# Performance work log

Hardware: AMD Instinct MI355X
Metric: run time of the kernel (lower is better)

## Reference

```python
import jax, jax.numpy as jnp
import numpy as np

MAXLEN = 256          # max per-graph segment length (static for jit)
SOFT_LABEL_NUM = 4    # hardcoded in the original module
B = 512               # num_graphs


def setup_inputs() -> dict:
    key = jax.random.key(0)
    k1, k2, k3 = jax.random.split(key, 3)
    # ragged per-graph lengths in [2, MAXLEN]; >=2 so the original's
    # length-1 skip path (and its cursor bug) never triggers
    s_num = jax.random.randint(k1, (B,), 2, MAXLEN + 1, dtype=jnp.int32)
    T = int(jnp.sum(s_num))
    logits = jax.random.normal(k2, (T,), dtype=jnp.float32)
    labels = jax.random.randint(k3, (T,), 0, SOFT_LABEL_NUM, dtype=jnp.int32)
    return {"logits": logits, "labels": labels, "s_num": s_num}


def reference(logits, labels, s_num):
    T = logits.shape[0]
    ends = jnp.cumsum(s_num)
    offsets = ends - s_num                                   # segment starts
    pos_in_seg = jnp.arange(MAXLEN)
    idx = jnp.clip(offsets[:, None] + pos_in_seg[None, :], 0, T - 1)  # [B, L]
    tok_mask = pos_in_seg[None, :] < s_num[:, None]                    # [B, L]

    lg = logits[idx]                                   # [B, L] padded logits
    lb = labels[idx]                                   # [B, L] padded labels

    # pairwise logsigmoid(pos - neg), computed once for all soft labels
    ls = jax.nn.log_sigmoid(lg[:, :, None] - lg[:, None, :])  # [B, L, L]

    means, valids = [], []
    for s in range(1, SOFT_LABEL_NUM):
        pos = (tok_mask & (lb == s)).astype(lg.dtype)  # [B, L]
        neg = (tok_mask & (lb < s)).astype(lg.dtype)   # [B, L]
        npos = pos.sum(-1)                             # [B]
        nneg = neg.sum(-1)                             # [B]
        pair_sum = jnp.einsum('bp,bpn,bn->b', pos, ls, neg)
        valid = (npos > 0) & (nneg > 0)
        mean_s = jnp.where(valid, pair_sum / jnp.maximum(npos * nneg, 1.0), 0.0)
        means.append(mean_s)
        valids.append(valid)

    means = jnp.stack(means)                 # [3, B]
    valids = jnp.stack(valids)               # [3, B]
    cnt = valids.astype(lg.dtype).sum(0)     # valid soft-label count per graph
    graph_valid = (s_num > 1) & (cnt > 0)
    graph_lp = jnp.where(graph_valid, means.sum(0) / jnp.maximum(cnt, 1.0), 0.0)
    n_valid = jnp.maximum(graph_valid.astype(lg.dtype).sum(), 1.0)
    loss = -(graph_lp.sum() / n_valid)
    return loss
```

## Files before the change

### kernel.cpp

```cpp
#include <hip/hip_runtime.h>
#include <hip/hip_bf16.h>


#define TAGHI 0xC0FFEE42u

__global__ __launch_bounds__(512) void bpr_one(const float* __restrict__ logits,
                                               const int* __restrict__ labels,
                                               const int* __restrict__ s_num,
                                               int B,
                                               unsigned long long* __restrict__ slot,
                                               float* __restrict__ out) {
    const int g    = blockIdx.x;
    const int t    = threadIdx.x;
    const int r    = t & 255;
    const int sl   = t >> 8;
    const int w    = t >> 6;
    const int lane = t & 63;

    __shared__ __align__(16) float se[256];
    __shared__ float sx[256];
    __shared__ float psum[4];
    __shared__ int   wcnt[4][4];
    __shared__ int   wpart[8];

    if (t < 4) psum[t] = 0.0f;

    int partial = 0;
    for (int i = t; i < g; i += 512) partial += s_num[i];
    #pragma unroll
    for (int off = 32; off > 0; off >>= 1)
        partial += __shfl_down(partial, off, 64);
    if (lane == 0) wpart[w] = partial;
    __syncthreads();
    int offset = 0;
    #pragma unroll
    for (int k = 0; k < 8; ++k) offset += wpart[k];
    const int L = s_num[g];

    float x = 0.0f;
    int   l = -1;
    if (t < 256 && t < L) {
        x = logits[offset + t];
        l = labels[offset + t];
    }
    const unsigned long long m0 = __ballot(l == 0);
    const unsigned long long m1 = __ballot(l == 1);
    const unsigned long long m2 = __ballot(l == 2);
    const unsigned long long m3 = __ballot(l == 3);
    if (w < 4 && lane == 0) {
        wcnt[w][0] = __popcll(m0);
        wcnt[w][1] = __popcll(m1);
        wcnt[w][2] = __popcll(m2);
        wcnt[w][3] = __popcll(m3);
    }
    const unsigned long long below = lane ? (~0ull >> (64 - lane)) : 0ull;
    const unsigned long long mymask =
        (l == 0) ? m0 : (l == 1) ? m1 : (l == 2) ? m2 : m3;
    const int rank = __popcll(mymask & below);
    __syncthreads();

    const int c0 = wcnt[0][0] + wcnt[1][0] + wcnt[2][0] + wcnt[3][0];
    const int c1 = wcnt[0][1] + wcnt[1][1] + wcnt[2][1] + wcnt[3][1];
    const int c2 = wcnt[0][2] + wcnt[1][2] + wcnt[2][2] + wcnt[3][2];
    const int c3 = wcnt[0][3] + wcnt[1][3] + wcnt[2][3] + wcnt[3][3];
    const int P1 = c0, P2 = c0 + c1, P3 = c0 + c1 + c2;

    if (t < 256 && t < L) {
        int base = (l == 0) ? 0 : (l == 1) ? P1 : (l == 2) ? P2 : P3;
        for (int w2 = 0; w2 < w; ++w2) base += wcnt[w2][l];
        const int pos = base + rank;
        se[pos] = __expf(x);
        sx[pos] = x;
    }
    __syncthreads();

    int si = 0;
    if (r < L) si = (r >= P1) + (r >= P2) + (r >= P3);
    const int C = (si == 1) ? P1 : (si == 2) ? P2 : (si == 3) ? P3 : 0;
    const float xi = sx[r];
    const float Ei = se[r];

    float acc2 = 0.0f;
    for (int j = 8 * sl; j + 8 <= C; j += 16) {
        const float4 e0 = *reinterpret_cast<const float4*>(&se[j]);
        const float4 e1 = *reinterpret_cast<const float4*>(&se[j + 4]);
        acc2 += __log2f(Ei + e0.x) + __log2f(Ei + e0.y)
              + __log2f(Ei + e0.z) + __log2f(Ei + e0.w)
              + __log2f(Ei + e1.x) + __log2f(Ei + e1.y)
              + __log2f(Ei + e1.z) + __log2f(Ei + e1.w);
    }
    const int jb = C & ~7;
    if (si > 0 && sl == ((C >> 3) & 1)) {
        for (int j = jb; j < C; ++j) acc2 += __log2f(Ei + se[j]);
    }
    float v = -0.69314718055994531f * acc2;
    if (sl == 0 && si > 0) v += (float)C * xi;

    #pragma unroll
    for (int s2 = 1; s2 < 4; ++s2) {
        float val = (si == s2) ? v : 0.0f;
        #pragma unroll
        for (int off = 32; off > 0; off >>= 1)
            val += __shfl_down(val, off, 64);
        if (lane == 0 && val != 0.0f) atomicAdd(&psum[s2], val);
    }
    __syncthreads();

    if (t == 0) {
        float lp = 0.0f;
        int   cc = 0;
        if (c1 > 0 && P1 > 0) { lp += psum[1] / ((float)c1 * (float)P1); ++cc; }
        if (c2 > 0 && P2 > 0) { lp += psum[2] / ((float)c2 * (float)P2); ++cc; }
        if (c3 > 0 && P3 > 0) { lp += psum[3] / ((float)c3 * (float)P3); ++cc; }
        const bool gv = (cc > 0);
        const float glp = gv ? lp / (float)cc : 0.0f;
        const unsigned int hi = (TAGHI & ~1u) | (gv ? 1u : 0u);
        const unsigned long long payload =
            ((unsigned long long)hi << 32) | (unsigned long long)__float_as_uint(glp);
        atomicExch(&slot[g], payload);
    }

    if (g == B - 1) {
        float s = 0.0f, n = 0.0f;
        for (int i = t; i < B; i += 512) {
            unsigned long long v2;
            for (;;) {
                v2 = atomicAdd(&slot[i], 0ull);
                if (((unsigned int)(v2 >> 32) & ~1u) == (TAGHI & ~1u)) break;
                __builtin_amdgcn_s_sleep(2);
            }
            s += __uint_as_float((unsigned int)v2);
            n += (float)((unsigned int)(v2 >> 32) & 1u);
        }
        #pragma unroll
        for (int off = 32; off > 0; off >>= 1) {
            s += __shfl_down(s, off, 64);
            n += __shfl_down(n, off, 64);
        }
        __syncthreads();
        if (lane == 0) { se[w] = s; sx[w] = n; }
        __syncthreads();
        if (t == 0) {
            float S = 0.0f, N = 0.0f;
            #pragma unroll
            for (int k = 0; k < 8; ++k) { S += se[k]; N += sx[k]; }
            out[0] = -(S / fmaxf(N, 1.0f));
        }
    }
}

extern "C" void kernel_launch(void* const* d_in, const int* in_sizes, int n_in,
                              void* d_out, int out_size, void* d_ws, size_t ws_size,
                              hipStream_t stream) {
    const float* logits = (const float*)d_in[0];
    const int*   labels = (const int*)d_in[1];
    const int*   s_num  = (const int*)d_in[2];
    int B = in_sizes[2];

    unsigned long long* slot = (unsigned long long*)d_ws;

    bpr_one<<<B, 512, 0, stream>>>(logits, labels, s_num, B,
                                   slot, (float*)d_out);
}
```

Baseline: 11.69 us.

## Process two graphs per block, one per 256-thread half, halving grid size

Each 512-thread block now handles two consecutive graphs, with each half of the block owning one graph and computing all pairwise terms for its rows alone, instead of splitting one graph's inner loop across two halves. This halves the number of blocks, the prefix-sum work over s_num, and the slot entries the last block must spin-wait on and reduce. The slot payload now packs a per-block valid-graph count under a 24-bit tag. The trade-off is that each thread's inner loop is up to twice as long, and the two halves can be unevenly loaded when graph lengths differ.

Measured after the change: 12.63 us. +8.1%, slower.

```diff
diff --git a/kernel.cpp b/kernel.cpp
--- a/kernel.cpp
+++ b/kernel.cpp
@@ -2,52 +2,61 @@
 #include <hip/hip_bf16.h>
 
 
-#define TAGHI 0xC0FFEE42u
+#define TAG24 0xC0FFEEu
 
 __global__ __launch_bounds__(512) void bpr_one(const float* __restrict__ logits,
                                                const int* __restrict__ labels,
                                                const int* __restrict__ s_num,
-                                               int B,
+                                               int B, int nb,
                                                unsigned long long* __restrict__ slot,
                                                float* __restrict__ out) {
-    const int g    = blockIdx.x;
+    const int b    = blockIdx.x;
     const int t    = threadIdx.x;
+    const int h    = t >> 8;
     const int r    = t & 255;
-    const int sl   = t >> 8;
     const int w    = t >> 6;
     const int lane = t & 63;
 
-    __shared__ __align__(16) float se[256];
-    __shared__ float sx[256];
-    __shared__ float psum[4];
-    __shared__ int   wcnt[4][4];
+    __shared__ __align__(16) float se[2][256];
+    __shared__ float sx[2][256];
+    __shared__ float psum[2][4];
+    __shared__ int   wcnt[8][4];
     __shared__ int   wpart[8];
+    __shared__ float hlp[2];
+    __shared__ int   hgv[2];
 
-    if (t < 4) psum[t] = 0.0f;
+    if (t < 8) psum[t >> 2][t & 3] = 0.0f;
+
+    const int gA = 2 * b;
+    const int gB = gA + 1;
 
     int partial = 0;
-    for (int i = t; i < g; i += 512) partial += s_num[i];
+    for (int i = t; i < gA; i += 512) partial += s_num[i];
     #pragma unroll
     for (int off = 32; off > 0; off >>= 1)
         partial += __shfl_down(partial, off, 64);
     if (lane == 0) wpart[w] = partial;
     __syncthreads();
-    int offset = 0;
+    int offsetA = 0;
     #pragma unroll
-    for (int k = 0; k < 8; ++k) offset += wpart[k];
-    const int L = s_num[g];
+    for (int k = 0; k < 8; ++k) offsetA += wpart[k];
+
+    const int LA = s_num[gA];
+    const int LB = (gB < B) ? s_num[gB] : 0;
+    const int L     = h ? LB : LA;
+    const int myoff = offsetA + (h ? LA : 0);
 
     float x = 0.0f;
     int   l = -1;
-    if (t < 256 && t < L) {
-        x = logits[offset + t];
-        l = labels[offset + t];
+    if (r < L) {
+        x = logits[myoff + r];
+        l = labels[myoff + r];
     }
     const unsigned long long m0 = __ballot(l == 0);
     const unsigned long long m1 = __ballot(l == 1);
     const unsigned long long m2 = __ballot(l == 2);
     const unsigned long long m3 = __ballot(l == 3);
-    if (w < 4 && lane == 0) {
+    if (lane == 0) {
         wcnt[w][0] = __popcll(m0);
         wcnt[w][1] = __popcll(m1);
         wcnt[w][2] = __popcll(m2);
@@ -59,42 +68,43 @@
     const int rank = __popcll(mymask & below);
     __syncthreads();
 
-    const int c0 = wcnt[0][0] + wcnt[1][0] + wcnt[2][0] + wcnt[3][0];
-    const int c1 = wcnt[0][1] + wcnt[1][1] + wcnt[2][1] + wcnt[3][1];
-    const int c2 = wcnt[0][2] + wcnt[1][2] + wcnt[2][2] + wcnt[3][2];
-    const int c3 = wcnt[0][3] + wcnt[1][3] + wcnt[2][3] + wcnt[3][3];
+    const int wb = h << 2;
+    const int c0 = wcnt[wb][0] + wcnt[wb+1][0] + wcnt[wb+2][0] + wcnt[wb+3][0];
+    const int c1 = wcnt[wb][1] + wcnt[wb+1][1] + wcnt[wb+2][1] + wcnt[wb+3][1];
+    const int c2 = wcnt[wb][2] + wcnt[wb+1][2] + wcnt[wb+2][2] + wcnt[wb+3][2];
+    const int c3 = wcnt[wb][3] + wcnt[wb+1][3] + wcnt[wb+2][3] + wcnt[wb+3][3];
     const int P1 = c0, P2 = c0 + c1, P3 = c0 + c1 + c2;
 
-    if (t < 256 && t < L) {
+    if (r < L) {
         int base = (l == 0) ? 0 : (l == 1) ? P1 : (l == 2) ? P2 : P3;
-        for (int w2 = 0; w2 < w; ++w2) base += wcnt[w2][l];
+        for (int w2 = wb; w2 < w; ++w2) base += wcnt[w2][l];
         const int pos = base + rank;
-        se[pos] = __expf(x);
-        sx[pos] = x;
+        se[h][pos] = __expf(x);
+        sx[h][pos] = x;
     }
     __syncthreads();
 
     int si = 0;
     if (r < L) si = (r >= P1) + (r >= P2) + (r >= P3);
     const int C = (si == 1) ? P1 : (si == 2) ? P2 : (si == 3) ? P3 : 0;
-    const float xi = sx[r];
-    const float Ei = se[r];
+    const float xi = sx[h][r];
+    const float Ei = se[h][r];
+    const float* seh = se[h];
 
     float acc2 = 0.0f;
-    for (int j = 8 * sl; j + 8 <= C; j += 16) {
-        const float4 e0 = *reinterpret_cast<const float4*>(&se[j]);
-        const float4 e1 = *reinterpret_cast<const float4*>(&se[j + 4]);
+    int j = 0;
+    for (; j + 8 <= C; j += 8) {
+        const float4 e0 = *reinterpret_cast<const float4*>(&seh[j]);
+        const float4 e1 = *reinterpret_cast<const float4*>(&seh[j + 4]);
         acc2 += __log2f(Ei + e0.x) + __log2f(Ei + e0.y)
               + __log2f(Ei + e0.z) + __log2f(Ei + e0.w)
               + __log2f(Ei + e1.x) + __log2f(Ei + e1.y)
               + __log2f(Ei + e1.z) + __log2f(Ei + e1.w);
     }
-    const int jb = C & ~7;
-    if (si > 0 && sl == ((C >> 3) & 1)) {
-        for (int j = jb; j < C; ++j) acc2 += __log2f(Ei + se[j]);
-    }
-    float v = -0.69314718055994531f * acc2;
-    if (sl == 0 && si > 0) v += (float)C * xi;
+    for (; j < C; ++j) acc2 += __log2f(Ei + seh[j]);
+
+    const float v = (si > 0)
+        ? (float)C * xi - 0.69314718055994531f * acc2 : 0.0f;
 
     #pragma unroll
     for (int s2 = 1; s2 < 4; ++s2) {
@@ -102,35 +112,42 @@
         #pragma unroll
         for (int off = 32; off > 0; off >>= 1)
             val += __shfl_down(val, off, 64);
-        if (lane == 0 && val != 0.0f) atomicAdd(&psum[s2], val);
+        if (lane == 0 && val != 0.0f) atomicAdd(&psum[h][s2], val);
+    }
+    __syncthreads();
+
+    if (r == 0) {
+        float lp = 0.0f;
+        int   cc = 0;
+        if (c1 > 0 && P1 > 0) { lp += psum[h][1] / ((float)c1 * (float)P1); ++cc; }
+        if (c2 > 0 && P2 > 0) { lp += psum[h][2] / ((float)c2 * (float)P2); ++cc; }
+        if (c3 > 0 && P3 > 0) { lp += psum[h][3] / ((float)c3 * (float)P3); ++cc; }
+        const bool gv = (cc > 0);
+        hlp[h] = gv ? lp / (float)cc : 0.0f;
+        hgv[h] = gv ? 1 : 0;
     }
     __syncthreads();
 
     if (t == 0) {
-        float lp = 0.0f;
-        int   cc = 0;
-        if (c1 > 0 && P1 > 0) { lp += psum[1] / ((float)c1 * (float)P1); ++cc; }
-        if (c2 > 0 && P2 > 0) { lp += psum[2] / ((float)c2 * (float)P2); ++cc; }
-        if (c3 > 0 && P3 > 0) { lp += psum[3] / ((float)c3 * (float)P3); ++cc; }
-        const bool gv = (cc > 0);
-        const float glp = gv ? lp / (float)cc : 0.0f;
-        const unsigned int hi = (TAGHI & ~1u) | (gv ? 1u : 0u);
+        const float S = hlp[0] + hlp[1];
+        const unsigned int N = (unsigned int)(hgv[0] + hgv[1]);
         const unsigned long long payload =
-            ((unsigned long long)hi << 32) | (unsigned long long)__float_as_uint(glp);
-        atomicExch(&slot[g], payload);
+            ((unsigned long long)((TAG24 << 8) | N) << 32)
+            | (unsigned long long)__float_as_uint(S);
+        atomicExch(&slot[b], payload);
     }
 
-    if (g == B - 1) {
+    if (b == nb - 1) {
         float s = 0.0f, n = 0.0f;
-        for (int i = t; i < B; i += 512) {
+        for (int i = t; i < nb; i += 512) {
             unsigned long long v2;
             for (;;) {
                 v2 = atomicAdd(&slot[i], 0ull);
-                if (((unsigned int)(v2 >> 32) & ~1u) == (TAGHI & ~1u)) break;
+                if ((unsigned int)(v2 >> 40) == TAG24) break;
                 __builtin_amdgcn_s_sleep(2);
             }
             s += __uint_as_float((unsigned int)v2);
-            n += (float)((unsigned int)(v2 >> 32) & 1u);
+            n += (float)((v2 >> 32) & 0xFFu);
         }
         #pragma unroll
         for (int off = 32; off > 0; off >>= 1) {
@@ -138,12 +155,12 @@
             n += __shfl_down(n, off, 64);
         }
         __syncthreads();
-        if (lane == 0) { se[w] = s; sx[w] = n; }
+        if (lane == 0) { se[0][w] = s; sx[0][w] = n; }
         __syncthreads();
         if (t == 0) {
             float S = 0.0f, N = 0.0f;
             #pragma unroll
-            for (int k = 0; k < 8; ++k) { S += se[k]; N += sx[k]; }
+            for (int k = 0; k < 8; ++k) { S += se[0][k]; N += sx[0][k]; }
             out[0] = -(S / fmaxf(N, 1.0f));
         }
     }
@@ -156,9 +173,10 @@
     const int*   labels = (const int*)d_in[1];
     const int*   s_num  = (const int*)d_in[2];
     int B = in_sizes[2];
+    int nb = (B + 1) / 2;
 
     unsigned long long* slot = (unsigned long long*)d_ws;
 
-    bpr_one<<<B, 512, 0, stream>>>(logits, labels, s_num, B,
-                                   slot, (float*)d_out);
+    bpr_one<<<nb, 512, 0, stream>>>(logits, labels, s_num, B, nb,
+                                    slot, (float*)d_out);
 }
```
